# Kernel optimization log

Measured on AMD Instinct MI355X. Metric: run time of the kernel, lower is better.

Reference implementation:

```python
import jax, jax.numpy as jnp
import numpy as np

DIM = 768
NUM_HEADS = 12
HEAD_DIM = DIM // NUM_HEADS
SCALE = HEAD_DIM ** -0.5
N, B = 1024, 8


def setup_inputs() -> dict:
    key = jax.random.key(0)
    ks = jax.random.split(key, 10)
    s = 0.02
    return {
        "q": jax.random.normal(ks[0], (N, B, DIM), jnp.float32),
        "k": jax.random.normal(ks[1], (N, B, DIM), jnp.float32),
        "v": jax.random.normal(ks[2], (N, B, DIM), jnp.float32),
        "v_img": jax.random.normal(ks[3], (N, B, DIM), jnp.float32),
        "Wq": jax.random.normal(ks[4], (DIM, DIM), jnp.float32) * s,
        "Wk": jax.random.normal(ks[5], (DIM, DIM), jnp.float32) * s,
        "Wv": jax.random.normal(ks[6], (DIM, DIM), jnp.float32) * s,
        "Wvim": jax.random.normal(ks[7], (DIM, DIM), jnp.float32) * s,
        "Wp": jax.random.normal(ks[8], (DIM, DIM), jnp.float32) * s,
        "bp": jnp.zeros((DIM,), jnp.float32),
        "Wpi": jax.random.normal(ks[9], (DIM, DIM), jnp.float32) * s,
        "bpi": jnp.zeros((DIM,), jnp.float32),
    }


def _heads(x):
    # [B, N, C] -> [B, H, N, Dh]
    b, n, _ = x.shape
    return x.reshape(b, n, NUM_HEADS, HEAD_DIM).transpose(0, 2, 1, 3)


def _merge(x):
    # [B, H, N, Dh] -> [B, N, C]
    b, h, n, d = x.shape
    return x.transpose(0, 2, 1, 3).reshape(b, n, h * d)


def reference(q, k, v, v_img, Wq, Wk, Wv, Wvim, Wp, bp, Wpi, bpi):
    # seq-first [N, B, C] -> batch-first [B, N, C]
    qb = jnp.transpose(q, (1, 0, 2)) @ Wq.T
    kb = jnp.transpose(k, (1, 0, 2)) @ Wk.T
    vb = jnp.transpose(v, (1, 0, 2)) @ Wv.T
    vib = jnp.transpose(v_img, (1, 0, 2)) @ Wvim.T

    qh, kh, vh, vih = _heads(qb), _heads(kb), _heads(vb), _heads(vib)

    # shared attention matrix, reused for both value streams
    attn = jnp.einsum("bhqd,bhkd->bhqk", qh, kh) * SCALE
    attn = jax.nn.softmax(attn, axis=-1)

    x = _merge(jnp.einsum("bhqk,bhkd->bhqd", attn, vh)) @ Wp.T + bp
    x_im = _merge(jnp.einsum("bhqk,bhkd->bhqd", attn, vih)) @ Wpi.T + bpi
    return (x, x_im)
```

## Files before the change

kernel.cpp:

```cpp
#include <hip/hip_runtime.h>

#define NSEQ 1024
#define BATCH 8
#define DIMC 768
#define NH 12
#define HD 64
#define SEG 6291456
#define WSEG 589824

typedef __attribute__((ext_vector_type(4))) float f32x4;
typedef __attribute__((ext_vector_type(4))) unsigned u32x4;
typedef __attribute__((ext_vector_type(8))) short s16x8;
typedef __attribute__((ext_vector_type(8))) __bf16 bf16x8;

#define GLL16(gsrc, ldst) __builtin_amdgcn_global_load_lds( \
    (const __attribute__((address_space(1))) unsigned int*)(const void*)(gsrc), \
    (__attribute__((address_space(3))) unsigned int*)(void*)(ldst), 16, 0, 0)

__device__ __forceinline__ short f2bf(float f) {
  union { float f; unsigned u; } v; v.f = f;
  unsigned r = (v.u + 0x7FFFu + ((v.u >> 16) & 1u)) >> 16;
  return (short)r;
}

__device__ __forceinline__ short f2bf1(float f) {
  unsigned r;
  asm("v_cvt_pk_bf16_f32 %0, %1, %2" : "=v"(r) : "v"(f), "v"(0.f));
  return (short)r;
}

__device__ __forceinline__ unsigned cvtpk(float lo, float hi) {
  unsigned r;
  asm("v_cvt_pk_bf16_f32 %0, %1, %2" : "=v"(r) : "v"(lo), "v"(hi));
  return r;
}

__device__ __forceinline__ f32x4 mfma16(bf16x8 a, bf16x8 b, f32x4 c) {
  return __builtin_amdgcn_mfma_f32_16x16x32_bf16(a, b, c, 0, 0, 0);
}

__global__ __launch_bounds__(256) void k_cvt4(
    const float* __restrict__ a0, const float* __restrict__ a1,
    const float* __restrict__ a2, const float* __restrict__ a3,
    short* __restrict__ b0, short* __restrict__ b1,
    short* __restrict__ b2, short* __restrict__ b3, int n4,
    float s0, float s1, float s2, float s3) {
  const float* src; short* dst; float sc;
  switch (blockIdx.y) {
    case 0: src = a0; dst = b0; sc = s0; break;
    case 1: src = a1; dst = b1; sc = s1; break;
    case 2: src = a2; dst = b2; sc = s2; break;
    default: src = a3; dst = b3; sc = s3; break;
  }
  int i = blockIdx.x * 256 + threadIdx.x;
  if (i >= n4) return;
  float4 f = reinterpret_cast<const float4*>(src)[i];
  short4 o;
  o.x = f2bf(f.x * sc); o.y = f2bf(f.y * sc); o.z = f2bf(f.z * sc); o.w = f2bf(f.w * sc);
  reinterpret_cast<short4*>(dst)[i] = o;
}

__global__ __launch_bounds__(256) void k_proj(
    const short* __restrict__ x0, const short* __restrict__ x1,
    const short* __restrict__ x2, const short* __restrict__ x3,
    const short* __restrict__ w0, const short* __restrict__ w1,
    const short* __restrict__ w2, const short* __restrict__ w3,
    short* __restrict__ y0, short* __restrict__ y1,
    short* __restrict__ y2, short* __restrict__ y3) {
  __shared__ __align__(16) short SM[32768];
  const int tid = threadIdx.x;
  const int lane = tid & 63;
  const int w = tid >> 6;
  const int wm = w >> 1, wn = w & 1;
  const int mt = blockIdx.x, nt = blockIdx.y, s = blockIdx.z;
  const short *X, *W; short* Y;
  if (s == 0)      { X = x0; W = w0; Y = y0; }
  else if (s == 1) { X = x1; W = w1; Y = y1; }
  else if (s == 2) { X = x2; W = w2; Y = y2; }
  else             { X = x3; W = w3; Y = y3; }

  f32x4 acc[4][4];
#pragma unroll
  for (int mi = 0; mi < 4; ++mi)
#pragma unroll
    for (int ni = 0; ni < 4; ++ni) acc[mi][ni] = (f32x4){0.f, 0.f, 0.f, 0.f};

#define PROJ_STAGE(BUF, KT) do { \
  _Pragma("unroll") for (int ii = 0; ii < 4; ++ii) { \
    int g = ii * 256 + tid; \
    int o = g * 16; \
    int r = o >> 7; \
    int c0 = ((o & 127) ^ ((r & 7) << 4)) >> 1; \
    int m = mt * 128 + r; \
    GLL16(X + ((size_t)((m & 1023) * BATCH + (m >> 10))) * DIMC + (KT) * 64 + c0, \
          (char*)(SM + (BUF) * 8192) + o); \
    GLL16(W + (size_t)(nt * 128 + r) * DIMC + (KT) * 64 + c0, \
          (char*)(SM + 16384 + (BUF) * 8192) + o); \
  } \
} while (0)

  PROJ_STAGE(0, 0);
  __syncthreads();
  int buf = 0;
  for (int kt = 0; kt < 12; ++kt) {
    if (kt < 11) PROJ_STAGE(buf ^ 1, kt + 1);
    const char* As = (const char*)(SM + buf * 8192);
    const char* Bs = (const char*)(SM + 16384 + buf * 8192);
#pragma unroll
    for (int kk = 0; kk < 2; ++kk) {
      bf16x8 a[4], b[4];
      int ce = kk * 32 + (lane >> 4) * 8;
#pragma unroll
      for (int mi = 0; mi < 4; ++mi) {
        int ra = wm * 64 + mi * 16 + (lane & 15);
        int byte = ((ra << 7) + (ce << 1)) ^ ((ra & 7) << 4);
        a[mi] = *(const bf16x8*)(As + byte);
      }
#pragma unroll
      for (int ni = 0; ni < 4; ++ni) {
        int rb = wn * 64 + ni * 16 + (lane & 15);
        int byte = ((rb << 7) + (ce << 1)) ^ ((rb & 7) << 4);
        b[ni] = *(const bf16x8*)(Bs + byte);
      }
#pragma unroll
      for (int mi = 0; mi < 4; ++mi)
#pragma unroll
        for (int ni = 0; ni < 4; ++ni)
          acc[mi][ni] = mfma16(a[mi], b[ni], acc[mi][ni]);
    }
    __syncthreads();
    buf ^= 1;
  }
#undef PROJ_STAGE

  if (s < 2) {
#pragma unroll
    for (int mi = 0; mi < 4; ++mi)
#pragma unroll
      for (int ni = 0; ni < 4; ++ni)
#pragma unroll
        for (int j = 0; j < 4; ++j) {
          int m = mt * 128 + wm * 64 + mi * 16 + (lane >> 4) * 4 + j;
          int dc = nt * 128 + wn * 64 + ni * 16 + (lane & 15);
          int b_ = m >> 10, n_ = m & 1023;
          int h_ = dc >> 6, d_ = dc & 63;
          Y[((size_t)(b_ * NH + h_) * NSEQ + n_) * HD + d_] = f2bf(acc[mi][ni][j]);
        }
  } else {
    __syncthreads();
    short* Ts = SM;
#pragma unroll
    for (int mi = 0; mi < 4; ++mi)
#pragma unroll
      for (int ni = 0; ni < 4; ++ni)
#pragma unroll
        for (int j = 0; j < 4; ++j) {
          int lm = wm * 64 + mi * 16 + (lane >> 4) * 4 + j;
          int ldc = wn * 64 + ni * 16 + (lane & 15);
          int swc = ldc ^ (lm & 126);
          Ts[lm * 128 + swc] = f2bf(acc[mi][ni][j]);
        }
    __syncthreads();
    int l2 = lane * 2;
#pragma unroll 4
    for (int it = 0; it < 32; ++it) {
      int ldc = it * 4 + w;
      short2 pk;
      pk.x = Ts[l2 * 128 + (ldc ^ (l2 & 126))];
      pk.y = Ts[(l2 + 1) * 128 + (ldc ^ ((l2 + 1) & 126))];
      int dc = nt * 128 + ldc;
      int h_ = dc >> 6, d_ = dc & 63;
      int m = mt * 128 + l2;
      int b_ = m >> 10, n_ = m & 1023;
      *(short2*)(Y + ((size_t)(b_ * NH + h_) * HD + d_) * NSEQ + n_) = pk;
    }
  }
}

__global__ __launch_bounds__(256) void k_attn(
    const short* __restrict__ qh, const short* __restrict__ kh,
    const short* __restrict__ vt, const short* __restrict__ vit,
    short* __restrict__ xo, short* __restrict__ xio) {
  __shared__ __align__(16) short Ks[2][4096];
  __shared__ __align__(16) short Vs[2][4096];
  __shared__ __align__(16) short Vis[2][4096];

  const int tid = threadIdx.x;
  const int lane = tid & 63;
  const int w = tid >> 6;
  const int blk = blockIdx.x;
  const int virt = (blk & 7) * 96 + (blk >> 3);
  const int bh = virt >> 3;
  const int qt = virt & 7;

  const short* qbase = qh + ((size_t)bh * NSEQ + qt * 128 + w * 32) * HD;
  bf16x8 qf[2][2];
#pragma unroll
  for (int mi = 0; mi < 2; ++mi)
#pragma unroll
    for (int kq = 0; kq < 2; ++kq)
      qf[mi][kq] = *(const bf16x8*)(qbase + (mi * 16 + (lane & 15)) * HD + kq * 32 + (lane >> 4) * 8);

  bf16x8 onesf;
#pragma unroll
  for (int i = 0; i < 8; ++i) onesf[i] = (__bf16)1.0f;

  f32x4 o_[2][4], oi_[2][4], l_acc[2];
#pragma unroll
  for (int mi = 0; mi < 2; ++mi) {
    l_acc[mi] = (f32x4){0.f, 0.f, 0.f, 0.f};
#pragma unroll
    for (int x = 0; x < 4; ++x) {
      o_[mi][x] = (f32x4){0.f, 0.f, 0.f, 0.f};
      oi_[mi][x] = (f32x4){0.f, 0.f, 0.f, 0.f};
    }
  }

  const short* khb = kh + (size_t)bh * NSEQ * HD;
  const short* vtb = vt + (size_t)bh * NSEQ * HD;
  const short* vitb = vit + (size_t)bh * NSEQ * HD;

#define ATTN_STAGE(BUF, KT) do { \
  _Pragma("unroll") for (int ii = 0; ii < 2; ++ii) { \
    int g = ii * 256 + tid; \
    int o = g * 16; \
    int r = o >> 7; \
    int c0 = ((o & 127) ^ ((r & 7) << 4)) >> 1; \
    GLL16(khb + (size_t)((KT) * 64 + r) * HD + c0, (char*)&Ks[BUF][0] + o); \
    GLL16(vtb + (size_t)r * NSEQ + (KT) * 64 + c0, (char*)&Vs[BUF][0] + o); \
    GLL16(vitb + (size_t)r * NSEQ + (KT) * 64 + c0, (char*)&Vis[BUF][0] + o); \
  } \
} while (0)

  ATTN_STAGE(0, 0);
  __syncthreads();
  int buf = 0;
  for (int kt = 0; kt < 16; ++kt) {
    if (kt < 15) ATTN_STAGE(buf ^ 1, kt + 1);
    const char* KsB = (const char*)&Ks[buf][0];
    const char* VsB = (const char*)&Vs[buf][0];
    const char* VisB = (const char*)&Vis[buf][0];

    unsigned pk0[2][4], pk1[2][4];
#pragma unroll
    for (int ni = 0; ni < 4; ++ni) {
      f32x4 s0 = (f32x4){0.f, 0.f, 0.f, 0.f};
      f32x4 s1 = (f32x4){0.f, 0.f, 0.f, 0.f};
#pragma unroll
      for (int kk = 0; kk < 2; ++kk) {
        int ce = kk * 32 + (lane >> 4) * 8;
        int rb = ni * 16 + (lane & 15);
        int byte = ((rb << 7) + (ce << 1)) ^ ((rb & 7) << 4);
        bf16x8 kfr = *(const bf16x8*)(KsB + byte);
        s0 = mfma16(kfr, qf[0][kk], s0);
        s1 = mfma16(kfr, qf[1][kk], s1);
      }
      pk0[0][ni] = cvtpk(exp2f(s0[0]), exp2f(s0[1]));
      pk1[0][ni] = cvtpk(exp2f(s0[2]), exp2f(s0[3]));
      pk0[1][ni] = cvtpk(exp2f(s1[0]), exp2f(s1[1]));
      pk1[1][ni] = cvtpk(exp2f(s1[2]), exp2f(s1[3]));
    }

    bf16x8 pa[2][2];
#pragma unroll
    for (int mi = 0; mi < 2; ++mi)
#pragma unroll
      for (int slot = 0; slot < 2; ++slot) {
        unsigned a0 = pk0[mi][2 * slot], a1 = pk0[mi][2 * slot + 1];
        asm("v_permlane32_swap_b32 %0, %1" : "+v"(a0), "+v"(a1));
        asm("v_permlane16_swap_b32 %0, %1" : "+v"(a0), "+v"(a1));
        unsigned b0 = pk1[mi][2 * slot], b1 = pk1[mi][2 * slot + 1];
        asm("v_permlane32_swap_b32 %0, %1" : "+v"(b0), "+v"(b1));
        asm("v_permlane16_swap_b32 %0, %1" : "+v"(b0), "+v"(b1));
        u32x4 pw = (u32x4){a0, b0, a1, b1};
        pa[mi][slot] = __builtin_bit_cast(bf16x8, pw);
      }

#pragma unroll
    for (int kk = 0; kk < 2; ++kk) {
      int co = kk * 32 + (lane >> 4) * 8;
      l_acc[0] = mfma16(pa[0][kk], onesf, l_acc[0]);
      l_acc[1] = mfma16(pa[1][kk], onesf, l_acc[1]);
#pragma unroll
      for (int nd = 0; nd < 4; ++nd) {
        int rv = nd * 16 + (lane & 15);
        int byte = ((rv << 7) + (co << 1)) ^ ((rv & 7) << 4);
        bf16x8 vb = *(const bf16x8*)(VsB + byte);
        bf16x8 vib = *(const bf16x8*)(VisB + byte);
        o_[0][nd] = mfma16(pa[0][kk], vb, o_[0][nd]);
        o_[1][nd] = mfma16(pa[1][kk], vb, o_[1][nd]);
        oi_[0][nd] = mfma16(pa[0][kk], vib, oi_[0][nd]);
        oi_[1][nd] = mfma16(pa[1][kk], vib, oi_[1][nd]);
      }
    }
    __syncthreads();
    buf ^= 1;
  }
#undef ATTN_STAGE

#pragma unroll
  for (int mi = 0; mi < 2; ++mi)
#pragma unroll
    for (int j = 0; j < 4; ++j) {
      float inv = 1.0f / l_acc[mi][j];
      int n_ = qt * 128 + w * 32 + mi * 16 + (lane >> 4) * 4 + j;
      size_t base = ((size_t)bh * NSEQ + n_) * HD;
#pragma unroll
      for (int nd = 0; nd < 4; ++nd) {
        int d_ = nd * 16 + (lane & 15);
        xo[base + d_] = f2bf1(o_[mi][nd][j] * inv);
        xio[base + d_] = f2bf1(oi_[mi][nd][j] * inv);
      }
    }
}

__global__ __launch_bounds__(256) void k_outproj(
    const short* __restrict__ xa, const short* __restrict__ xb,
    const short* __restrict__ wa, const short* __restrict__ wb,
    const float* __restrict__ ba, const float* __restrict__ bb,
    float* __restrict__ out) {
  __shared__ __align__(16) short SM[32768];
  const int tid = threadIdx.x;
  const int lane = tid & 63;
  const int w = tid >> 6;
  const int wm = w >> 1, wn = w & 1;
  const int mt = blockIdx.x, nt = blockIdx.y, s = blockIdx.z;
  const short* X = (s == 0) ? xa : xb;
  const short* W = (s == 0) ? wa : wb;
  const float* bias = (s == 0) ? ba : bb;
  float* O = out + (size_t)s * SEG;

  f32x4 acc[4][4];
#pragma unroll
  for (int mi = 0; mi < 4; ++mi)
#pragma unroll
    for (int ni = 0; ni < 4; ++ni) acc[mi][ni] = (f32x4){0.f, 0.f, 0.f, 0.f};

#define OUTP_STAGE(BUF, KT) do { \
  _Pragma("unroll") for (int ii = 0; ii < 4; ++ii) { \
    int g = ii * 256 + tid; \
    int o = g * 16; \
    int r = o >> 7; \
    int c0 = ((o & 127) ^ ((r & 7) << 4)) >> 1; \
    int m = mt * 128 + r; \
    GLL16(X + (((size_t)(m >> 10) * NH + (KT)) * NSEQ + (m & 1023)) * HD + c0, \
          (char*)(SM + (BUF) * 8192) + o); \
    GLL16(W + (size_t)(nt * 128 + r) * DIMC + (KT) * 64 + c0, \
          (char*)(SM + 16384 + (BUF) * 8192) + o); \
  } \
} while (0)

  OUTP_STAGE(0, 0);
  __syncthreads();
  int buf = 0;
  for (int kt = 0; kt < 12; ++kt) {
    if (kt < 11) OUTP_STAGE(buf ^ 1, kt + 1);
    const char* As = (const char*)(SM + buf * 8192);
    const char* Bs = (const char*)(SM + 16384 + buf * 8192);
#pragma unroll
    for (int kk = 0; kk < 2; ++kk) {
      bf16x8 a[4], b[4];
      int ce = kk * 32 + (lane >> 4) * 8;
#pragma unroll
      for (int mi = 0; mi < 4; ++mi) {
        int ra = wm * 64 + mi * 16 + (lane & 15);
        int byte = ((ra << 7) + (ce << 1)) ^ ((ra & 7) << 4);
        a[mi] = *(const bf16x8*)(As + byte);
      }
#pragma unroll
      for (int ni = 0; ni < 4; ++ni) {
        int rb = wn * 64 + ni * 16 + (lane & 15);
        int byte = ((rb << 7) + (ce << 1)) ^ ((rb & 7) << 4);
        b[ni] = *(const bf16x8*)(Bs + byte);
      }
#pragma unroll
      for (int mi = 0; mi < 4; ++mi)
#pragma unroll
        for (int ni = 0; ni < 4; ++ni)
          acc[mi][ni] = mfma16(a[mi], b[ni], acc[mi][ni]);
    }
    __syncthreads();
    buf ^= 1;
  }
#undef OUTP_STAGE

#pragma unroll
  for (int mi = 0; mi < 4; ++mi)
#pragma unroll
    for (int ni = 0; ni < 4; ++ni)
#pragma unroll
      for (int j = 0; j < 4; ++j) {
        int m = mt * 128 + wm * 64 + mi * 16 + (lane >> 4) * 4 + j;
        int dc = nt * 128 + wn * 64 + ni * 16 + (lane & 15);
        O[(size_t)m * DIMC + dc] = acc[mi][ni][j] + bias[dc];
      }
}

extern "C" void kernel_launch(void* const* d_in, const int* in_sizes, int n_in,
                              void* d_out, int out_size, void* d_ws, size_t ws_size,
                              hipStream_t stream) {
  (void)in_sizes; (void)n_in; (void)out_size; (void)ws_size;
  const float* q    = (const float*)d_in[0];
  const float* k    = (const float*)d_in[1];
  const float* v    = (const float*)d_in[2];
  const float* vimg = (const float*)d_in[3];
  const float* Wq   = (const float*)d_in[4];
  const float* Wk   = (const float*)d_in[5];
  const float* Wv   = (const float*)d_in[6];
  const float* Wvim = (const float*)d_in[7];
  const float* Wp   = (const float*)d_in[8];
  const float* bp   = (const float*)d_in[9];
  const float* Wpi  = (const float*)d_in[10];
  const float* bpi  = (const float*)d_in[11];

  short* ws = (short*)d_ws;
  short* xq  = ws;
  short* xk  = ws + (size_t)SEG;
  short* xv  = ws + (size_t)2 * SEG;
  short* xvi = ws + (size_t)3 * SEG;
  short* wqb  = ws + (size_t)4 * SEG;
  short* wkb  = wqb + WSEG;
  short* wvb  = wkb + WSEG;
  short* wvib = wvb + WSEG;
  short* wpb  = wvib + WSEG;
  short* wpib = wpb + WSEG;
  short* qh  = ws + (size_t)4 * SEG + 6 * (size_t)WSEG;
  short* kh  = qh + (size_t)SEG;
  short* vht = kh + (size_t)SEG;
  short* viht = vht + (size_t)SEG;
  short* xo  = viht + (size_t)SEG;
  short* xio = xo + (size_t)SEG;

  const float SCL2E = 0.125f * 1.44269504f;

  k_cvt4<<<dim3(SEG / 4 / 256, 4), 256, 0, stream>>>(q, k, v, vimg, xq, xk, xv, xvi, SEG / 4,
                                                     1.f, 1.f, 1.f, 1.f);
  k_cvt4<<<dim3(WSEG / 4 / 256, 4), 256, 0, stream>>>(Wq, Wk, Wv, Wvim, wqb, wkb, wvb, wvib, WSEG / 4,
                                                      SCL2E, 1.f, 1.f, 1.f);
  k_cvt4<<<dim3(WSEG / 4 / 256, 2), 256, 0, stream>>>(Wp, Wpi, Wp, Wpi, wpb, wpib, wpb, wpib, WSEG / 4,
                                                      1.f, 1.f, 1.f, 1.f);

  k_proj<<<dim3(64, 6, 4), 256, 0, stream>>>(xq, xk, xv, xvi, wqb, wkb, wvb, wvib, qh, kh, vht, viht);

  k_attn<<<dim3(768), 256, 0, stream>>>(qh, kh, vht, viht, xo, xio);

  k_outproj<<<dim3(64, 6, 2), 256, 0, stream>>>(xo, xio, wpb, wpib, bp, bpi, (float*)d_out);
}
```

Before: 314.1 us.

## Single-buffer B tiles in projection GEMMs with vmcnt-based waits, merge weight conversions

The projection and output-projection GEMMs now keep only one B (weight) tile in shared memory instead of two. Each iteration issues the current B load and the next A prefetch, then waits with explicit s_waitcnt vmcnt and raw s_barrier in place of __syncthreads. This cuts LDS per block from 64KB to 48KB, which may allow more resident blocks, at the cost of exposing B-load latency on every iteration. The two weight-conversion launches are merged into one six-way kernel, and epilogue conversions use the hardware bf16 pack instruction.

Measured after the change: 316.7 us. About the same (+0.8%).

```diff
diff --git a/kernel.cpp b/kernel.cpp
--- a/kernel.cpp
+++ b/kernel.cpp
@@ -39,18 +39,47 @@
   return __builtin_amdgcn_mfma_f32_16x16x32_bf16(a, b, c, 0, 0, 0);
 }
 
+#define WAITVM(N) asm volatile("s_waitcnt vmcnt(" #N ")" ::: "memory")
+#define SBAR() do { __builtin_amdgcn_sched_barrier(0); \
+                    __builtin_amdgcn_s_barrier(); \
+                    __builtin_amdgcn_sched_barrier(0); } while (0)
+
 __global__ __launch_bounds__(256) void k_cvt4(
     const float* __restrict__ a0, const float* __restrict__ a1,
     const float* __restrict__ a2, const float* __restrict__ a3,
     short* __restrict__ b0, short* __restrict__ b1,
-    short* __restrict__ b2, short* __restrict__ b3, int n4,
-    float s0, float s1, float s2, float s3) {
-  const float* src; short* dst; float sc;
+    short* __restrict__ b2, short* __restrict__ b3, int n4) {
+  const float* src; short* dst;
   switch (blockIdx.y) {
-    case 0: src = a0; dst = b0; sc = s0; break;
-    case 1: src = a1; dst = b1; sc = s1; break;
-    case 2: src = a2; dst = b2; sc = s2; break;
-    default: src = a3; dst = b3; sc = s3; break;
+    case 0: src = a0; dst = b0; break;
+    case 1: src = a1; dst = b1; break;
+    case 2: src = a2; dst = b2; break;
+    default: src = a3; dst = b3; break;
+  }
+  int i = blockIdx.x * 256 + threadIdx.x;
+  if (i >= n4) return;
+  float4 f = reinterpret_cast<const float4*>(src)[i];
+  short4 o;
+  o.x = f2bf(f.x); o.y = f2bf(f.y); o.z = f2bf(f.z); o.w = f2bf(f.w);
+  reinterpret_cast<short4*>(dst)[i] = o;
+}
+
+__global__ __launch_bounds__(256) void k_cvtw(
+    const float* __restrict__ a0, const float* __restrict__ a1,
+    const float* __restrict__ a2, const float* __restrict__ a3,
+    const float* __restrict__ a4, const float* __restrict__ a5,
+    short* __restrict__ b0, short* __restrict__ b1,
+    short* __restrict__ b2, short* __restrict__ b3,
+    short* __restrict__ b4, short* __restrict__ b5,
+    int n4, float sc0) {
+  const float* src; short* dst; float sc = 1.f;
+  switch (blockIdx.y) {
+    case 0: src = a0; dst = b0; sc = sc0; break;
+    case 1: src = a1; dst = b1; break;
+    case 2: src = a2; dst = b2; break;
+    case 3: src = a3; dst = b3; break;
+    case 4: src = a4; dst = b4; break;
+    default: src = a5; dst = b5; break;
   }
   int i = blockIdx.x * 256 + threadIdx.x;
   if (i >= n4) return;
@@ -67,7 +96,7 @@
     const short* __restrict__ w2, const short* __restrict__ w3,
     short* __restrict__ y0, short* __restrict__ y1,
     short* __restrict__ y2, short* __restrict__ y3) {
-  __shared__ __align__(16) short SM[32768];
+  __shared__ __align__(16) short SM[24576];
   const int tid = threadIdx.x;
   const int lane = tid & 63;
   const int w = tid >> 6;
@@ -85,7 +114,7 @@
 #pragma unroll
     for (int ni = 0; ni < 4; ++ni) acc[mi][ni] = (f32x4){0.f, 0.f, 0.f, 0.f};
 
-#define PROJ_STAGE(BUF, KT) do { \
+#define STAGE_A(BUF, KT) do { \
   _Pragma("unroll") for (int ii = 0; ii < 4; ++ii) { \
     int g = ii * 256 + tid; \
     int o = g * 16; \
@@ -94,18 +123,28 @@
     int m = mt * 128 + r; \
     GLL16(X + ((size_t)((m & 1023) * BATCH + (m >> 10))) * DIMC + (KT) * 64 + c0, \
           (char*)(SM + (BUF) * 8192) + o); \
-    GLL16(W + (size_t)(nt * 128 + r) * DIMC + (KT) * 64 + c0, \
-          (char*)(SM + 16384 + (BUF) * 8192) + o); \
   } \
 } while (0)
-
-  PROJ_STAGE(0, 0);
-  __syncthreads();
+#define STAGE_B(KT) do { \
+  _Pragma("unroll") for (int ii = 0; ii < 4; ++ii) { \
+    int g = ii * 256 + tid; \
+    int o = g * 16; \
+    int r = o >> 7; \
+    int c0 = ((o & 127) ^ ((r & 7) << 4)) >> 1; \
+    GLL16(W + (size_t)(nt * 128 + r) * DIMC + (KT) * 64 + c0, \
+          (char*)(SM + 16384) + o); \
+  } \
+} while (0)
+
+  STAGE_A(0, 0);
   int buf = 0;
   for (int kt = 0; kt < 12; ++kt) {
-    if (kt < 11) PROJ_STAGE(buf ^ 1, kt + 1);
+    STAGE_B(kt);
+    if (kt < 11) { STAGE_A(buf ^ 1, kt + 1); WAITVM(4); }
+    else         { WAITVM(0); }
+    SBAR();
     const char* As = (const char*)(SM + buf * 8192);
-    const char* Bs = (const char*)(SM + 16384 + buf * 8192);
+    const char* Bs = (const char*)(SM + 16384);
 #pragma unroll
     for (int kk = 0; kk < 2; ++kk) {
       bf16x8 a[4], b[4];
@@ -128,10 +167,11 @@
         for (int ni = 0; ni < 4; ++ni)
           acc[mi][ni] = mfma16(a[mi], b[ni], acc[mi][ni]);
     }
-    __syncthreads();
+    SBAR();
     buf ^= 1;
   }
-#undef PROJ_STAGE
+#undef STAGE_A
+#undef STAGE_B
 
   if (s < 2) {
 #pragma unroll
@@ -144,10 +184,9 @@
           int dc = nt * 128 + wn * 64 + ni * 16 + (lane & 15);
           int b_ = m >> 10, n_ = m & 1023;
           int h_ = dc >> 6, d_ = dc & 63;
-          Y[((size_t)(b_ * NH + h_) * NSEQ + n_) * HD + d_] = f2bf(acc[mi][ni][j]);
+          Y[((size_t)(b_ * NH + h_) * NSEQ + n_) * HD + d_] = f2bf1(acc[mi][ni][j]);
         }
   } else {
-    __syncthreads();
     short* Ts = SM;
 #pragma unroll
     for (int mi = 0; mi < 4; ++mi)
@@ -158,7 +197,7 @@
           int lm = wm * 64 + mi * 16 + (lane >> 4) * 4 + j;
           int ldc = wn * 64 + ni * 16 + (lane & 15);
           int swc = ldc ^ (lm & 126);
-          Ts[lm * 128 + swc] = f2bf(acc[mi][ni][j]);
+          Ts[lm * 128 + swc] = f2bf1(acc[mi][ni][j]);
         }
     __syncthreads();
     int l2 = lane * 2;
@@ -319,7 +358,7 @@
     const short* __restrict__ wa, const short* __restrict__ wb,
     const float* __restrict__ ba, const float* __restrict__ bb,
     float* __restrict__ out) {
-  __shared__ __align__(16) short SM[32768];
+  __shared__ __align__(16) short SM[24576];
   const int tid = threadIdx.x;
   const int lane = tid & 63;
   const int w = tid >> 6;
@@ -336,7 +375,7 @@
 #pragma unroll
     for (int ni = 0; ni < 4; ++ni) acc[mi][ni] = (f32x4){0.f, 0.f, 0.f, 0.f};
 
-#define OUTP_STAGE(BUF, KT) do { \
+#define STAGE_A(BUF, KT) do { \
   _Pragma("unroll") for (int ii = 0; ii < 4; ++ii) { \
     int g = ii * 256 + tid; \
     int o = g * 16; \
@@ -345,18 +384,28 @@
     int m = mt * 128 + r; \
     GLL16(X + (((size_t)(m >> 10) * NH + (KT)) * NSEQ + (m & 1023)) * HD + c0, \
           (char*)(SM + (BUF) * 8192) + o); \
-    GLL16(W + (size_t)(nt * 128 + r) * DIMC + (KT) * 64 + c0, \
-          (char*)(SM + 16384 + (BUF) * 8192) + o); \
   } \
 } while (0)
-
-  OUTP_STAGE(0, 0);
-  __syncthreads();
+#define STAGE_B(KT) do { \
+  _Pragma("unroll") for (int ii = 0; ii < 4; ++ii) { \
+    int g = ii * 256 + tid; \
+    int o = g * 16; \
+    int r = o >> 7; \
+    int c0 = ((o & 127) ^ ((r & 7) << 4)) >> 1; \
+    GLL16(W + (size_t)(nt * 128 + r) * DIMC + (KT) * 64 + c0, \
+          (char*)(SM + 16384) + o); \
+  } \
+} while (0)
+
+  STAGE_A(0, 0);
   int buf = 0;
   for (int kt = 0; kt < 12; ++kt) {
-    if (kt < 11) OUTP_STAGE(buf ^ 1, kt + 1);
+    STAGE_B(kt);
+    if (kt < 11) { STAGE_A(buf ^ 1, kt + 1); WAITVM(4); }
+    else         { WAITVM(0); }
+    SBAR();
     const char* As = (const char*)(SM + buf * 8192);
-    const char* Bs = (const char*)(SM + 16384 + buf * 8192);
+    const char* Bs = (const char*)(SM + 16384);
 #pragma unroll
     for (int kk = 0; kk < 2; ++kk) {
       bf16x8 a[4], b[4];
@@ -379,10 +428,11 @@
         for (int ni = 0; ni < 4; ++ni)
           acc[mi][ni] = mfma16(a[mi], b[ni], acc[mi][ni]);
     }
-    __syncthreads();
+    SBAR();
     buf ^= 1;
   }
-#undef OUTP_STAGE
+#undef STAGE_A
+#undef STAGE_B
 
 #pragma unroll
   for (int mi = 0; mi < 4; ++mi)
@@ -433,12 +483,10 @@
 
   const float SCL2E = 0.125f * 1.44269504f;
 
-  k_cvt4<<<dim3(SEG / 4 / 256, 4), 256, 0, stream>>>(q, k, v, vimg, xq, xk, xv, xvi, SEG / 4,
-                                                     1.f, 1.f, 1.f, 1.f);
-  k_cvt4<<<dim3(WSEG / 4 / 256, 4), 256, 0, stream>>>(Wq, Wk, Wv, Wvim, wqb, wkb, wvb, wvib, WSEG / 4,
-                                                      SCL2E, 1.f, 1.f, 1.f);
-  k_cvt4<<<dim3(WSEG / 4 / 256, 2), 256, 0, stream>>>(Wp, Wpi, Wp, Wpi, wpb, wpib, wpb, wpib, WSEG / 4,
-                                                      1.f, 1.f, 1.f, 1.f);
+  k_cvt4<<<dim3(SEG / 4 / 256, 4), 256, 0, stream>>>(q, k, v, vimg, xq, xk, xv, xvi, SEG / 4);
+  k_cvtw<<<dim3(WSEG / 4 / 256, 6), 256, 0, stream>>>(Wq, Wk, Wv, Wvim, Wp, Wpi,
+                                                      wqb, wkb, wvb, wvib, wpb, wpib,
+                                                      WSEG / 4, SCL2E);
 
   k_proj<<<dim3(64, 6, 4), 256, 0, stream>>>(xq, xk, xv, xvi, wqb, wkb, wvb, wvib, qh, kh, vht, viht);
 
```
